# Performance work log

Measured on AMD Instinct MI355X. Metric: run time of the kernel, lower is better.

The kernel has to match this reference:

```python
import jax, jax.numpy as jnp
import numpy as np

N = 2048      # nodes
E = 65536     # edges (avg degree 32)
NV = 6        # n_views (edge_attr dim)
C1, C2, C3 = 32, 32, 32


def _nnconv(x, edge_index, edge_attr, W, b, root, bias, in_c, out_c):
    # Edge MLP: Linear(n_views, in*out) + ReLU -> per-edge weight matrix [E, in, out]
    w = jax.nn.relu(edge_attr @ W + b).reshape(-1, in_c, out_c)
    src, dst = edge_index[0], edge_index[1]  # source_to_target flow
    msg = jnp.einsum('ei,eio->eo', x[src], w)          # gather + edge-specific matmul
    summed = jax.ops.segment_sum(msg, dst, num_segments=N)
    cnt = jax.ops.segment_sum(jnp.ones((msg.shape[0],), x.dtype), dst, num_segments=N)
    agg = summed / jnp.maximum(cnt, 1.0)[:, None]       # scatter-mean (0 for isolated nodes)
    return agg + x @ root + bias                        # root weight + bias (PyG NNConv defaults)


def setup_inputs() -> dict:
    key = jax.random.key(0)
    ks = jax.random.split(key, 12)
    s = 0.1
    return {
        'x': jax.random.normal(ks[0], (N, 1), jnp.float32),
        'edge_attr': jax.random.uniform(ks[1], (E, NV), jnp.float32),
        'edge_index': jax.random.randint(ks[2], (2, E), 0, N, jnp.int64),
        'W1': jax.random.normal(ks[3], (NV, 1 * C1), jnp.float32) * s,
        'b1': jnp.zeros((1 * C1,), jnp.float32),
        'root1': jax.random.normal(ks[4], (1, C1), jnp.float32) * s,
        'bias1': jnp.zeros((C1,), jnp.float32),
        'W2': jax.random.normal(ks[5], (NV, C1 * C2), jnp.float32) * s,
        'b2': jnp.zeros((C1 * C2,), jnp.float32),
        'root2': jax.random.normal(ks[6], (C1, C2), jnp.float32) * s,
        'bias2': jnp.zeros((C2,), jnp.float32),
        'W3': jax.random.normal(ks[7], (NV, C2 * C3), jnp.float32) * s,
        'b3': jnp.zeros((C2 * C3,), jnp.float32),
        'root3': jax.random.normal(ks[8], (C2, C3), jnp.float32) * s,
        'bias3': jnp.zeros((C3,), jnp.float32),
    }


def reference(x, edge_attr, edge_index, W1, b1, root1, bias1, W2, b2, root2, bias2, W3, b3, root3, bias3):
    h = jax.nn.relu(_nnconv(x, edge_index, edge_attr, W1, b1, root1, bias1, 1, C1))
    h = jax.nn.relu(_nnconv(h, edge_index, edge_attr, W2, b2, root2, bias2, C1, C2))
    h = jax.nn.relu(_nnconv(h, edge_index, edge_attr, W3, b3, root3, bias3, C2, C3))
    # CBT: cbt[i, j] = sum_k |h[j, k] - h[i, k]|  (all-pairs L1 distance, [N, N])
    cbt = jnp.sum(jnp.abs(h[None, :, :] - h[:, None, :]), axis=2)
    return cbt
```

## Files before the change

kernel.cpp:

```cpp
#include <hip/hip_runtime.h>

#define N_NODES 2048
#define N_EDGES 65536
#define NV 6
#define C 32


__global__ void edge1_kernel(const float* __restrict__ x,
                             const float* __restrict__ ea,
                             const int* __restrict__ src,
                             const int* __restrict__ dst,
                             const float* __restrict__ W1,
                             const float* __restrict__ b1,
                             float* __restrict__ sum1,
                             float* __restrict__ cnt) {
    int t = blockIdx.x * blockDim.x + threadIdx.x;
    int e = t >> 5, o = t & 31;
    if (e >= N_EDGES) return;
    const float* eap = ea + e * NV;
    float w = b1[o];
#pragma unroll
    for (int v = 0; v < NV; v++) w = fmaf(eap[v], W1[v * C + o], w);
    w = fmaxf(w, 0.0f);
    int d = dst[e];
    atomicAdd(&sum1[d * C + o], x[src[e]] * w);
    if (o == 0) atomicAdd(&cnt[d], 1.0f);
}

template <int IN_C>
__global__ void node_kernel(const float* __restrict__ sum,
                            const float* __restrict__ cnt,
                            const float* __restrict__ hprev,
                            const float* __restrict__ root,
                            const float* __restrict__ bias,
                            float* __restrict__ hout) {
    int t = blockIdx.x * blockDim.x + threadIdx.x;
    int n = t >> 5, o = t & 31;
    float inv = 1.0f / fmaxf(cnt[n], 1.0f);
    float acc = sum[t] * inv + bias[o];
#pragma unroll
    for (int i = 0; i < IN_C; i++) acc = fmaf(hprev[n * IN_C + i], root[i * C + o], acc);
    hout[t] = fmaxf(acc, 0.0f);
}

__global__ __launch_bounds__(256) void edge23_kernel(
    const float* __restrict__ hprev,
    const float* __restrict__ ea,
    const int* __restrict__ src,
    const int* __restrict__ dst,
    const float* __restrict__ W,
    const float* __restrict__ b,
    float* __restrict__ sumout)
{
    __shared__ float hb[4][256];
    const int lane = threadIdx.x & 63;
    const int o = lane & 31;
    const int half = lane >> 5;
    const int i0 = half * 16;
    const int w = threadIdx.x >> 6;
    float* hbw = &hb[w][0];

    float wreg[16][6], breg[16];
#pragma unroll
    for (int j = 0; j < 16; j++) {
#pragma unroll
        for (int v = 0; v < 6; v++) wreg[j][v] = W[v * 1024 + (i0 + j) * C + o];
        breg[j] = b[(i0 + j) * C + o];
    }

    const int wid = (blockIdx.x * 256 + threadIdx.x) >> 6;
    for (int g = wid; g < N_EDGES / 8; g += 2048) {
        const int e0 = g * 8;
        const int4 sq = *(const int4*)&src[e0 + half * 4];
        float4 hq;
        hq.x = hprev[sq.x * C + o];
        hq.y = hprev[sq.y * C + o];
        hq.z = hprev[sq.z * C + o];
        hq.w = hprev[sq.w * C + o];
        *(float4*)&hbw[half * 128 + o * 4] = hq;

        float accs[8];
        const float4* eap4 = (const float4*)(ea + (size_t)e0 * NV);
#pragma unroll
        for (int sub = 0; sub < 2; sub++) {
            float eaf[24];
#pragma unroll
            for (int t = 0; t < 6; t++) *(float4*)&eaf[t * 4] = eap4[sub * 6 + t];
            float a0 = 0.0f, a1 = 0.0f, a2 = 0.0f, a3 = 0.0f;
#pragma unroll
            for (int j = 0; j < 16; j++) {
                const float4 hA = *(const float4*)&hbw[sub * 128 + (i0 + j) * 4];
                const float bb = breg[j];
                const float w0 = wreg[j][0], w1 = wreg[j][1], w2 = wreg[j][2];
                const float w3 = wreg[j][3], w4 = wreg[j][4], w5 = wreg[j][5];
                float t0 = bb, t1 = bb, t2 = bb, t3 = bb;
                t0 = fmaf(eaf[0],  w0, t0); t1 = fmaf(eaf[6],  w0, t1);
                t2 = fmaf(eaf[12], w0, t2); t3 = fmaf(eaf[18], w0, t3);
                t0 = fmaf(eaf[1],  w1, t0); t1 = fmaf(eaf[7],  w1, t1);
                t2 = fmaf(eaf[13], w1, t2); t3 = fmaf(eaf[19], w1, t3);
                t0 = fmaf(eaf[2],  w2, t0); t1 = fmaf(eaf[8],  w2, t1);
                t2 = fmaf(eaf[14], w2, t2); t3 = fmaf(eaf[20], w2, t3);
                t0 = fmaf(eaf[3],  w3, t0); t1 = fmaf(eaf[9],  w3, t1);
                t2 = fmaf(eaf[15], w3, t2); t3 = fmaf(eaf[21], w3, t3);
                t0 = fmaf(eaf[4],  w4, t0); t1 = fmaf(eaf[10], w4, t1);
                t2 = fmaf(eaf[16], w4, t2); t3 = fmaf(eaf[22], w4, t3);
                t0 = fmaf(eaf[5],  w5, t0); t1 = fmaf(eaf[11], w5, t1);
                t2 = fmaf(eaf[17], w5, t2); t3 = fmaf(eaf[23], w5, t3);
                a0 = fmaf(hA.x, fmaxf(t0, 0.0f), a0);
                a1 = fmaf(hA.y, fmaxf(t1, 0.0f), a1);
                a2 = fmaf(hA.z, fmaxf(t2, 0.0f), a2);
                a3 = fmaf(hA.w, fmaxf(t3, 0.0f), a3);
            }
            accs[sub * 4 + 0] = a0; accs[sub * 4 + 1] = a1;
            accs[sub * 4 + 2] = a2; accs[sub * 4 + 3] = a3;
        }
#pragma unroll
        for (int k = 0; k < 8; k++) accs[k] += __shfl_down(accs[k], 32);

        const int4 dA = *(const int4*)&dst[e0];
        const int4 dB = *(const int4*)&dst[e0 + 4];
        if (lane < 32) {
            atomicAdd(&sumout[dA.x * C + o], accs[0]);
            atomicAdd(&sumout[dA.y * C + o], accs[1]);
            atomicAdd(&sumout[dA.z * C + o], accs[2]);
            atomicAdd(&sumout[dA.w * C + o], accs[3]);
            atomicAdd(&sumout[dB.x * C + o], accs[4]);
            atomicAdd(&sumout[dB.y * C + o], accs[5]);
            atomicAdd(&sumout[dB.z * C + o], accs[6]);
            atomicAdd(&sumout[dB.w * C + o], accs[7]);
        }
    }
}

__global__ __launch_bounds__(256) void cbt_kernel(const float* __restrict__ h,
                                                  float* __restrict__ out) {
    __shared__ float hj_s[64][33];
    __shared__ float hi_s[64 * 32];
    const int lane = threadIdx.x & 63;
    const int w = threadIdx.x >> 6;
    const int j0 = blockIdx.x * 64;
    const int i0 = blockIdx.y * 64;
    for (int t = threadIdx.x; t < 64 * 32; t += 256) {
        hj_s[t >> 5][t & 31] = h[j0 * 32 + t];
        hi_s[t] = h[i0 * 32 + t];
    }
    __syncthreads();
    float hj[32];
#pragma unroll
    for (int k = 0; k < 32; k++) hj[k] = hj_s[lane][k];
    const int j = j0 + lane;
#pragma unroll 4
    for (int ii = w * 16; ii < w * 16 + 16; ii++) {
        float acc = 0.0f;
#pragma unroll
        for (int k = 0; k < 32; k++) {
            acc += fabsf(hi_s[ii * 32 + k] - hj[k]);
        }
        out[(size_t)(i0 + ii) * N_NODES + j] = acc;
    }
}

extern "C" void kernel_launch(void* const* d_in, const int* in_sizes, int n_in,
                              void* d_out, int out_size, void* d_ws, size_t ws_size,
                              hipStream_t stream) {
    const float* x         = (const float*)d_in[0];
    const float* edge_attr = (const float*)d_in[1];
    const int*   edge_idx  = (const int*)d_in[2];
    const float* W1 = (const float*)d_in[3];
    const float* b1 = (const float*)d_in[4];
    const float* root1 = (const float*)d_in[5];
    const float* bias1 = (const float*)d_in[6];
    const float* W2 = (const float*)d_in[7];
    const float* b2 = (const float*)d_in[8];
    const float* root2 = (const float*)d_in[9];
    const float* bias2 = (const float*)d_in[10];
    const float* W3 = (const float*)d_in[11];
    const float* b3 = (const float*)d_in[12];
    const float* root3 = (const float*)d_in[13];
    const float* bias3 = (const float*)d_in[14];

    const int* src = edge_idx;
    const int* dst = edge_idx + N_EDGES;

    float* ws   = (float*)d_ws;
    float* cnt  = ws;
    float* sum1 = ws + N_NODES;
    float* sum2 = sum1 + N_NODES * C;
    float* sum3 = sum2 + N_NODES * C;
    float* h1   = sum3 + N_NODES * C;
    float* h2   = h1 + N_NODES * C;
    float* h3   = h2 + N_NODES * C;

    hipMemsetAsync(d_ws, 0, (size_t)(N_NODES + 3 * N_NODES * C) * sizeof(float), stream);

    edge1_kernel<<<(N_EDGES * C) / 256, 256, 0, stream>>>(x, edge_attr, src, dst, W1, b1, sum1, cnt);
    node_kernel<1><<<(N_NODES * C) / 256, 256, 0, stream>>>(sum1, cnt, x, root1, bias1, h1);

    edge23_kernel<<<512, 256, 0, stream>>>(h1, edge_attr, src, dst, W2, b2, sum2);
    node_kernel<C><<<(N_NODES * C) / 256, 256, 0, stream>>>(sum2, cnt, h1, root2, bias2, h2);

    edge23_kernel<<<512, 256, 0, stream>>>(h2, edge_attr, src, dst, W3, b3, sum3);
    node_kernel<C><<<(N_NODES * C) / 256, 256, 0, stream>>>(sum3, cnt, h2, root3, bias3, h3);

    cbt_kernel<<<dim3(N_NODES / 64, N_NODES / 64), 256, 0, stream>>>(h3, (float*)d_out);
}
```

Before: 168.5 us.

## Restructure edge1 with shared staging, zero sums in-kernel, double edge23 grid

Edge1 now processes 32 edges per wavefront: it stages edge attributes and gathered source features in shared memory, keeps W1 in registers and drops the launch to 512 blocks. The same kernel also zeroes the sum2/sum3 buffers, which shrinks the memset. Edge23 gets a launch-bounds occupancy hint, a grid of 1024 blocks with a derived stride, and issues its dst loads earlier. Together these aim to cut redundant global loads, memset traffic and latency, at the cost of higher register pressure and more scheduling risk.

New measurement: 190.2 us. 1.13x slower.

```diff
diff --git a/kernel.cpp b/kernel.cpp
--- a/kernel.cpp
+++ b/kernel.cpp
@@ -4,27 +4,50 @@
 #define N_EDGES 65536
 #define NV 6
 #define C 32
-
-
-__global__ void edge1_kernel(const float* __restrict__ x,
-                             const float* __restrict__ ea,
-                             const int* __restrict__ src,
-                             const int* __restrict__ dst,
-                             const float* __restrict__ W1,
-                             const float* __restrict__ b1,
-                             float* __restrict__ sum1,
-                             float* __restrict__ cnt) {
-    int t = blockIdx.x * blockDim.x + threadIdx.x;
-    int e = t >> 5, o = t & 31;
-    if (e >= N_EDGES) return;
-    const float* eap = ea + e * NV;
-    float w = b1[o];
-#pragma unroll
-    for (int v = 0; v < NV; v++) w = fmaf(eap[v], W1[v * C + o], w);
-    w = fmaxf(w, 0.0f);
-    int d = dst[e];
-    atomicAdd(&sum1[d * C + o], x[src[e]] * w);
-    if (o == 0) atomicAdd(&cnt[d], 1.0f);
+#define BLK 256
+
+
+__global__ __launch_bounds__(BLK) void edge1_kernel(
+    const float* __restrict__ x, const float* __restrict__ ea,
+    const int* __restrict__ src, const int* __restrict__ dst,
+    const float* __restrict__ W1, const float* __restrict__ b1,
+    float* __restrict__ sum1, float* __restrict__ sum23,
+    float* __restrict__ cnt) {
+    __shared__ float ebuf[4][192];
+    __shared__ float xbuf[4][32];
+    const int tid = blockIdx.x * BLK + threadIdx.x;
+    sum23[tid] = 0.0f;
+    const int lane = threadIdx.x & 63;
+    const int o = lane & 31;
+    const int half = lane >> 5;
+    const int w = threadIdx.x >> 6;
+    const int e0 = (tid >> 6) * 32;
+
+    float w1r[NV];
+#pragma unroll
+    for (int v = 0; v < NV; v++) w1r[v] = W1[v * C + o];
+    const float b1o = b1[o];
+
+    if (lane < 48)
+        *(float4*)&ebuf[w][lane * 4] = ((const float4*)(ea + (size_t)e0 * NV))[lane];
+    if (lane < 32) xbuf[w][lane] = x[src[e0 + lane]];
+
+#pragma unroll 4
+    for (int k = 0; k < 16; k++) {
+        const int e = half * 16 + k;
+        const float* ep = &ebuf[w][e * 6];
+        float t = b1o;
+        t = fmaf(ep[0], w1r[0], t);
+        t = fmaf(ep[1], w1r[1], t);
+        t = fmaf(ep[2], w1r[2], t);
+        t = fmaf(ep[3], w1r[3], t);
+        t = fmaf(ep[4], w1r[4], t);
+        t = fmaf(ep[5], w1r[5], t);
+        const float m = xbuf[w][e] * fmaxf(t, 0.0f);
+        const int d = dst[e0 + e];
+        atomicAdd(&sum1[d * C + o], m);
+        if (o == 0) atomicAdd(&cnt[d], 1.0f);
+    }
 }
 
 template <int IN_C>
@@ -43,7 +66,7 @@
     hout[t] = fmaxf(acc, 0.0f);
 }
 
-__global__ __launch_bounds__(256) void edge23_kernel(
+__global__ __launch_bounds__(BLK, 3) void edge23_kernel(
     const float* __restrict__ hprev,
     const float* __restrict__ ea,
     const int* __restrict__ src,
@@ -68,10 +91,13 @@
         breg[j] = b[(i0 + j) * C + o];
     }
 
-    const int wid = (blockIdx.x * 256 + threadIdx.x) >> 6;
-    for (int g = wid; g < N_EDGES / 8; g += 2048) {
+    const int nw = (gridDim.x * BLK) >> 6;
+    const int wid = (blockIdx.x * BLK + threadIdx.x) >> 6;
+    for (int g = wid; g < N_EDGES / 8; g += nw) {
         const int e0 = g * 8;
         const int4 sq = *(const int4*)&src[e0 + half * 4];
+        const int4 dA = *(const int4*)&dst[e0];
+        const int4 dB = *(const int4*)&dst[e0 + 4];
         float4 hq;
         hq.x = hprev[sq.x * C + o];
         hq.y = hprev[sq.y * C + o];
@@ -116,9 +142,6 @@
         }
 #pragma unroll
         for (int k = 0; k < 8; k++) accs[k] += __shfl_down(accs[k], 32);
-
-        const int4 dA = *(const int4*)&dst[e0];
-        const int4 dB = *(const int4*)&dst[e0 + 4];
         if (lane < 32) {
             atomicAdd(&sumout[dA.x * C + o], accs[0]);
             atomicAdd(&sumout[dA.y * C + o], accs[1]);
@@ -132,7 +155,7 @@
     }
 }
 
-__global__ __launch_bounds__(256) void cbt_kernel(const float* __restrict__ h,
+__global__ __launch_bounds__(BLK) void cbt_kernel(const float* __restrict__ h,
                                                   float* __restrict__ out) {
     __shared__ float hj_s[64][33];
     __shared__ float hi_s[64 * 32];
@@ -140,7 +163,7 @@
     const int w = threadIdx.x >> 6;
     const int j0 = blockIdx.x * 64;
     const int i0 = blockIdx.y * 64;
-    for (int t = threadIdx.x; t < 64 * 32; t += 256) {
+    for (int t = threadIdx.x; t < 64 * 32; t += BLK) {
         hj_s[t >> 5][t & 31] = h[j0 * 32 + t];
         hi_s[t] = h[i0 * 32 + t];
     }
@@ -153,9 +176,7 @@
     for (int ii = w * 16; ii < w * 16 + 16; ii++) {
         float acc = 0.0f;
 #pragma unroll
-        for (int k = 0; k < 32; k++) {
-            acc += fabsf(hi_s[ii * 32 + k] - hj[k]);
-        }
+        for (int k = 0; k < 32; k++) acc += fabsf(hi_s[ii * 32 + k] - hj[k]);
         out[(size_t)(i0 + ii) * N_NODES + j] = acc;
     }
 }
@@ -191,16 +212,17 @@
     float* h2   = h1 + N_NODES * C;
     float* h3   = h2 + N_NODES * C;
 
-    hipMemsetAsync(d_ws, 0, (size_t)(N_NODES + 3 * N_NODES * C) * sizeof(float), stream);
-
-    edge1_kernel<<<(N_EDGES * C) / 256, 256, 0, stream>>>(x, edge_attr, src, dst, W1, b1, sum1, cnt);
-    node_kernel<1><<<(N_NODES * C) / 256, 256, 0, stream>>>(sum1, cnt, x, root1, bias1, h1);
-
-    edge23_kernel<<<512, 256, 0, stream>>>(h1, edge_attr, src, dst, W2, b2, sum2);
-    node_kernel<C><<<(N_NODES * C) / 256, 256, 0, stream>>>(sum2, cnt, h1, root2, bias2, h2);
-
-    edge23_kernel<<<512, 256, 0, stream>>>(h2, edge_attr, src, dst, W3, b3, sum3);
-    node_kernel<C><<<(N_NODES * C) / 256, 256, 0, stream>>>(sum3, cnt, h2, root3, bias3, h3);
-
-    cbt_kernel<<<dim3(N_NODES / 64, N_NODES / 64), 256, 0, stream>>>(h3, (float*)d_out);
-}
+    hipMemsetAsync(d_ws, 0, (size_t)(N_NODES + N_NODES * C) * sizeof(float), stream);
+
+    edge1_kernel<<<512, BLK, 0, stream>>>(x, edge_attr, src, dst, W1, b1,
+                                          sum1, sum2, cnt);
+    node_kernel<1><<<(N_NODES * C) / BLK, BLK, 0, stream>>>(sum1, cnt, x, root1, bias1, h1);
+
+    edge23_kernel<<<1024, BLK, 0, stream>>>(h1, edge_attr, src, dst, W2, b2, sum2);
+    node_kernel<C><<<(N_NODES * C) / BLK, BLK, 0, stream>>>(sum2, cnt, h1, root2, bias2, h2);
+
+    edge23_kernel<<<1024, BLK, 0, stream>>>(h2, edge_attr, src, dst, W3, b3, sum3);
+    node_kernel<C><<<(N_NODES * C) / BLK, BLK, 0, stream>>>(sum3, cnt, h2, root3, bias3, h3);
+
+    cbt_kernel<<<dim3(N_NODES / 64, N_NODES / 64), BLK, 0, stream>>>(h3, (float*)d_out);
+}
```
